# Kernel tuning notes

Measured on AMD Instinct MI355X. Metric: run time of the kernel, lower is better.

Reference implementation:

```python
import jax, jax.numpy as jnp
import numpy as np

SLOPE = 25.0          # fast_sigmoid surrogate slope
H_THRESH = 1.0        # hidden_threshold
O_THRESH = 1.0        # output_threshold
CH_THRESH = 1.0       # cochlea LIF threshold
W_MIN, W_MAX, BITS = 0.001, 1.0, 5

@jax.custom_vjp
def spike(v):
    return (v > 0).astype(v.dtype)

def _spike_fwd(v):
    return spike(v), v

def _spike_bwd(v, g):
    # fast_sigmoid surrogate gradient: 1 / (slope*|v| + 1)^2
    return (g / (SLOPE * jnp.abs(v) + 1.0) ** 2,)

spike.defvjp(_spike_fwd, _spike_bwd)

def fake_quant(w):
    # STE fake quantization (same forward value in train/eval)
    levels = 2 ** BITS
    scale = (W_MAX - W_MIN) / (levels - 1)
    wc = jnp.clip(w, W_MIN, W_MAX)
    q = jnp.round((wc - W_MIN) / scale) * scale + W_MIN
    return wc + jax.lax.stop_gradient(q - wc)

def lif(cur, mem, beta, thresh):
    # snnTorch Leaky, reset_mechanism='subtract': reset from previous mem (detached),
    # then integrate, then fire on new mem.
    reset = jax.lax.stop_gradient(spike(mem - thresh))
    mem = jnp.clip(beta, 0.0, 1.0) * mem + cur - reset * thresh
    spk = spike(mem - thresh)
    return spk, mem

def setup_inputs() -> dict:
    key = jax.random.key(0)
    ks = jax.random.split(key, 8)
    B, T, IN, HID, OUT = 64, 500, 256, 512, 35
    return {
        "x": jax.random.normal(ks[0], (B, T, 1), dtype=jnp.float32),
        "Wch": jax.random.normal(ks[1], (IN, 1), dtype=jnp.float32) * (1.0),
        "W1": jax.random.uniform(ks[2], (HID, IN), minval=W_MIN, maxval=W_MAX, dtype=jnp.float32),
        "W2": jax.random.uniform(ks[3], (HID, HID), minval=W_MIN, maxval=W_MAX, dtype=jnp.float32),
        "W3": jax.random.uniform(ks[4], (HID, HID), minval=W_MIN, maxval=W_MAX, dtype=jnp.float32),
        "W4": jax.random.uniform(ks[5], (OUT, HID), minval=W_MIN, maxval=W_MAX, dtype=jnp.float32),
        "cochlea_betas": jax.random.uniform(ks[6], (IN,), minval=0.05, maxval=0.99, dtype=jnp.float32),
        "beta1": jnp.float32(0.95),
        "beta2": jnp.float32(0.95),
        "beta3": jnp.float32(0.95),
        "beta4": jnp.float32(0.9),
    }

def reference(x, Wch, W1, W2, W3, W4, cochlea_betas, beta1, beta2, beta3, beta4):
    B = x.shape[0]
    # weights are static across time: quantize once, outside the scan
    q1, q2, q3, q4 = fake_quant(W1), fake_quant(W2), fake_quant(W3), fake_quant(W4)
    init = (
        jnp.zeros((B, Wch.shape[0]), x.dtype),  # ch_mem
        jnp.zeros((B, W1.shape[0]), x.dtype),   # mem1
        jnp.zeros((B, W2.shape[0]), x.dtype),   # mem2
        jnp.zeros((B, W3.shape[0]), x.dtype),   # mem3
        jnp.zeros((B, W4.shape[0]), x.dtype),   # mem4
    )

    def step(carry, xt):
        chm, m1, m2, m3, m4 = carry
        ch_spk, chm = lif(xt @ Wch.T, chm, cochlea_betas, CH_THRESH)
        s1, m1 = lif(ch_spk @ q1.T, m1, beta1, H_THRESH)
        s2, m2 = lif(s1 @ q2.T, m2, beta2, H_THRESH)
        s3, m3 = lif(s2 @ q3.T, m3, beta3, H_THRESH)
        s4, m4 = lif(s3 @ q4.T, m4, beta4, O_THRESH)
        return (chm, m1, m2, m3, m4), (s1, s2, s3, s4, m4)

    _, (spk1, spk2, spk3, spk4, mem4) = jax.lax.scan(step, init, jnp.swapaxes(x, 0, 1))
    # each is [T, B, features], matching torch.stack(..., dim=0)
    return spk1, spk2, spk3, spk4, mem4
```

## Files before the change

kernel.cpp:

```cpp
#include <hip/hip_runtime.h>
#include <stdint.h>

#define TT   500
#define BB   64
#define IND  256
#define HD   512
#define OD   35

typedef __attribute__((ext_vector_type(4))) int i32x4;

#define SCALE_F ((float)((1.0 - 0.001) / 31.0))

__device__ __forceinline__ void load16_lds(const int8_t* g, int8_t* l) {
  __builtin_amdgcn_global_load_lds((const __attribute__((address_space(1))) void*)g,
                                   (__attribute__((address_space(3))) void*)l, 16, 0, 0);
}

__global__ __launch_bounds__(256) void k_prep_cochlea(const float* __restrict__ W1,
                                                      const float* __restrict__ W2,
                                                      const float* __restrict__ W3,
                                                      const float* __restrict__ W4,
                                                      int8_t* __restrict__ wk1,
                                                      int8_t* __restrict__ wk2,
                                                      int8_t* __restrict__ wk3,
                                                      int8_t* __restrict__ wk4,
                                                      const float* __restrict__ x,
                                                      const float* __restrict__ Wch,
                                                      const float* __restrict__ cbetas,
                                                      int8_t* __restrict__ chs) {
  __shared__ float xs[TT];
  if (blockIdx.x < 2688) {
    int id = blockIdx.x * 256 + threadIdx.x;
    const float* W; int8_t* wk; int idx, K, H;
    if (id < 131072)       { idx = id;          W = W1; wk = wk1; K = 256; H = 512; }
    else if (id < 393216)  { idx = id - 131072; W = W2; wk = wk2; K = 512; H = 512; }
    else if (id < 655360)  { idx = id - 393216; W = W3; wk = wk3; K = 512; H = 512; }
    else                   { idx = id - 655360; W = W4; wk = wk4; K = 512; H = 35;  }
    int h = idx / K;
    int k = idx - h * K;
    int8_t bits = 0;
    if (h < H) {
      float w  = W[h * K + k];
      float wc = fminf(1.0f, fmaxf(0.001f, w));
      float v  = (wc - 0.001f) / SCALE_F;
      float q  = rintf(v);
      bits = (int8_t)q;
    }
    wk[idx] = bits;
  } else {
    int b = blockIdx.x - 2688;
    int i = threadIdx.x;
    for (int t = threadIdx.x; t < TT; t += 256) xs[t] = x[b * TT + t];
    __syncthreads();
    float w    = Wch[i];
    float beta = fminf(1.0f, fmaxf(0.0f, cbetas[i]));
    float mem  = 0.0f;
    for (int t = 0; t < TT; ++t) {
      float cur = __fmul_rn(xs[t], w);
      int   rs  = (mem > 1.0f);
      float t2  = __fadd_rn(__fmul_rn(beta, mem), cur);
      mem = rs ? __fsub_rn(t2, 1.0f) : t2;
      int spk = (mem > 1.0f);
      chs[(size_t)(t * BB + b) * IND + i] = (int8_t)spk;
    }
  }
}

template<int K>
__device__ __forceinline__ void stage_a(const int8_t* __restrict__ A, int8_t* As,
                                        int b, int gnext, int w, int lane) {
  constexpr int CH = K / 16;
  if (w > 0) {
    constexpr int per = (CH + 2) / 3;
    int jlo = (w - 1) * per, jhi = jlo + per; if (jhi > CH) jhi = CH;
    for (int j = jlo; j < jhi; ++j) {
      int L = j * 64 + lane;
      int r = L / CH, sl = L % CH;
      int kg = (sl - 5 * r) & (CH - 1);
      int t = gnext * 64 + r; if (t > 499) t = 499;
      load16_lds(A + ((size_t)t * 64 + b) * K + kg * 16, &As[j * 1024]);
    }
  }
}

template<int K, bool LAST>
__global__ __launch_bounds__(256, 2) void k_layer(const int8_t* __restrict__ A,
                                                  const int8_t* __restrict__ Bw,
                                                  const float* __restrict__ pbeta,
                                                  float* __restrict__ spk_out,
                                                  int8_t* __restrict__ s_out,
                                                  float* __restrict__ mem_out) {
  constexpr int CH = K / 16;
  constexpr int KS = K / 64;
  __shared__ __align__(16) int8_t Bs[64 * K];
  __shared__ __align__(16) int8_t As[64 * K];
  __shared__ float curbuf[64][64];
  int tid = threadIdx.x, lane = tid & 63, w = tid >> 6;
  int b, h0;
  if (LAST) { b = blockIdx.x;      h0 = 0; }
  else      { b = blockIdx.x & 63; h0 = (blockIdx.x >> 6) * 64; }
  float beta = fminf(1.0f, fmaxf(0.0f, *pbeta));
#pragma unroll
  for (int i = 0; i < CH / 4; ++i) {
    int L = i * 256 + tid;
    int row = L / CH, sl = L % CH;
    int kg = (sl - 5 * row) & (CH - 1);
    load16_lds(Bw + (size_t)(h0 + row) * K + kg * 16, &Bs[(i * 256 + w * 64) * 16]);
  }
  stage_a<K>(A, As, b, 0, w, lane);
  __syncthreads();
  const double DSCALE = (double)SCALE_F;
  const double DWMIN  = (double)0.001f;
  float mem = 0.0f;
  int lr = lane & 15, lk = lane >> 4;
  int arow = w * 16 + lr;
  i32x4 breg[4][KS];
#pragma unroll
  for (int cg = 0; cg < 4; ++cg)
#pragma unroll
    for (int ks = 0; ks < KS; ++ks) {
      int row = cg * 16 + lr;
      int s0 = (ks * 4 + lk + 5 * row) & (CH - 1);
      breg[cg][ks] = *(const i32x4*)&Bs[row * K + s0 * 16];
    }
  const i32x4 ones = {0x01010101, 0x01010101, 0x01010101, 0x01010101};
  for (int g = 0; g < 8; ++g) {
    i32x4 acc0 = {0,0,0,0}, acc1 = {0,0,0,0}, acc2 = {0,0,0,0}, acc3 = {0,0,0,0};
    i32x4 acc4 = {0,0,0,0};
#pragma unroll
    for (int ks = 0; ks < KS; ++ks) {
      int s0 = (ks * 4 + lk + 5 * arow) & (CH - 1);
      i32x4 av = *(const i32x4*)&As[arow * K + s0 * 16];
      acc0 = __builtin_amdgcn_mfma_i32_16x16x64_i8(av, breg[0][ks], acc0, 0, 0, 0);
      acc1 = __builtin_amdgcn_mfma_i32_16x16x64_i8(av, breg[1][ks], acc1, 0, 0, 0);
      acc2 = __builtin_amdgcn_mfma_i32_16x16x64_i8(av, breg[2][ks], acc2, 0, 0, 0);
      acc3 = __builtin_amdgcn_mfma_i32_16x16x64_i8(av, breg[3][ks], acc3, 0, 0, 0);
      acc4 = __builtin_amdgcn_mfma_i32_16x16x64_i8(av, ones, acc4, 0, 0, 0);
    }
    int pr = w * 16 + lk * 4;
#pragma unroll
    for (int i = 0; i < 4; ++i) {
      double nd = (double)acc4[i] * DWMIN;
      curbuf[pr + i][ 0 + lr] = (float)((double)acc0[i] * DSCALE + nd);
      curbuf[pr + i][16 + lr] = (float)((double)acc1[i] * DSCALE + nd);
      curbuf[pr + i][32 + lr] = (float)((double)acc2[i] * DSCALE + nd);
      curbuf[pr + i][48 + lr] = (float)((double)acc3[i] * DSCALE + nd);
    }
    __builtin_amdgcn_sched_barrier(0);
    asm volatile("s_waitcnt lgkmcnt(0)" ::: "memory");
    __builtin_amdgcn_s_barrier();
    __builtin_amdgcn_sched_barrier(0);
    if (g < 7) stage_a<K>(A, As, b, g + 1, w, lane);
    if (w == 0) {
      float curA[16], curB[16];
#define LOADQ(dst, q)                                                         \
      { _Pragma("unroll") for (int r = 0; r < 16; ++r)                        \
          dst[r] = curbuf[(q) * 16 + r][lane]; }
#define CHAINQ(src, q)                                                        \
      { _Pragma("unroll") for (int r = 0; r < 16; ++r) {                      \
          int t = g * 64 + (q) * 16 + r;                                      \
          int   rs = (mem > 1.0f);                                            \
          float t2 = __fadd_rn(__fmul_rn(beta, mem), src[r]);                 \
          mem = rs ? __fsub_rn(t2, 1.0f) : t2;                                \
          int spk = (mem > 1.0f);                                             \
          if (t < 500) {                                                      \
            int row = t * 64 + b;                                             \
            if (!LAST) {                                                      \
              __builtin_nontemporal_store(spk ? 1.0f : 0.0f,                  \
                  &spk_out[(size_t)t * 32768 + (b << 9) + h0 + lane]);        \
              s_out[(size_t)row * 512 + h0 + lane] = (int8_t)spk;             \
            } else if (lane < OD) {                                           \
              __builtin_nontemporal_store(spk ? 1.0f : 0.0f,                  \
                  &spk_out[(size_t)t * (BB * OD) + b * OD + lane]);           \
              __builtin_nontemporal_store(mem,                                \
                  &mem_out[(size_t)t * (BB * OD) + b * OD + lane]);           \
            }                                                                 \
          } } }
      LOADQ(curA, 0)
      LOADQ(curB, 1)
      CHAINQ(curA, 0)
      LOADQ(curA, 2)
      CHAINQ(curB, 1)
      LOADQ(curB, 3)
      CHAINQ(curA, 2)
      CHAINQ(curB, 3)
#undef LOADQ
#undef CHAINQ
    }
    __builtin_amdgcn_sched_barrier(0);
    if (w == 0) asm volatile("s_waitcnt lgkmcnt(0)" ::: "memory");
    else        asm volatile("s_waitcnt vmcnt(0) lgkmcnt(0)" ::: "memory");
    __builtin_amdgcn_s_barrier();
    __builtin_amdgcn_sched_barrier(0);
  }
}

extern "C" void kernel_launch(void* const* d_in, const int* in_sizes, int n_in,
                              void* d_out, int out_size, void* d_ws, size_t ws_size,
                              hipStream_t stream) {
  const float* x      = (const float*)d_in[0];
  const float* Wch    = (const float*)d_in[1];
  const float* W1     = (const float*)d_in[2];
  const float* W2     = (const float*)d_in[3];
  const float* W3     = (const float*)d_in[4];
  const float* W4     = (const float*)d_in[5];
  const float* cbetas = (const float*)d_in[6];
  const float* b1     = (const float*)d_in[7];
  const float* b2     = (const float*)d_in[8];
  const float* b3     = (const float*)d_in[9];
  const float* b4     = (const float*)d_in[10];

  uint8_t* ws = (uint8_t*)d_ws;
  int8_t*   wk1   = (int8_t*)(ws + 0);
  int8_t*   wk2   = (int8_t*)(ws + 131072);
  int8_t*   wk3   = (int8_t*)(ws + 393216);
  int8_t*   wk4   = (int8_t*)(ws + 655360);
  int8_t*   chs   = (int8_t*)(ws + 688128);
  int8_t*   sbufA = (int8_t*)(ws + 8880128);
  int8_t*   sbufB = (int8_t*)(ws + 25264128);

  float* out  = (float*)d_out;
  float* spk1 = out;
  float* spk2 = out + 16384000;
  float* spk3 = out + 32768000;
  float* spk4 = out + 49152000;
  float* mem4 = out + 50272000;

  k_prep_cochlea<<<2752, 256, 0, stream>>>(W1, W2, W3, W4, wk1, wk2, wk3, wk4,
                                           x, Wch, cbetas, chs);

  k_layer<256, false><<<512, 256, 0, stream>>>(chs,   wk1, b1, spk1, sbufA, nullptr);
  k_layer<512, false><<<512, 256, 0, stream>>>(sbufA, wk2, b2, spk2, sbufB, nullptr);
  k_layer<512, false><<<512, 256, 0, stream>>>(sbufB, wk3, b3, spk3, sbufA, nullptr);
  k_layer<512, true ><<<64,  256, 0, stream>>>(sbufA, wk4, b4, spk4, nullptr, mem4);
}
```

Measured before the change: 339.3 us.

## Specialize warps to overlap MFMA, LIF chain, and A-tile loads in layer kernel

The layer kernel grows from 4 to 8 waves and splits them by role. Wave 0 runs the serial LIF recurrence, waves 1-4 each compute a 32x32 MFMA tile of the next time-group's currents, and waves 5-7 prefetch the A tile two groups ahead. Before, the matrix multiply, the chain and the loads ran one after another within each time group. Now the scan of group g overlaps the GEMM of group g+1, at the cost of more barriers per iteration and a single shared current buffer that the barriers must protect.

```diff
diff --git a/kernel.cpp b/kernel.cpp
--- a/kernel.cpp
+++ b/kernel.cpp
@@ -70,21 +70,19 @@
 __device__ __forceinline__ void stage_a(const int8_t* __restrict__ A, int8_t* As,
                                         int b, int gnext, int w, int lane) {
   constexpr int CH = K / 16;
-  if (w > 0) {
-    constexpr int per = (CH + 2) / 3;
-    int jlo = (w - 1) * per, jhi = jlo + per; if (jhi > CH) jhi = CH;
-    for (int j = jlo; j < jhi; ++j) {
-      int L = j * 64 + lane;
-      int r = L / CH, sl = L % CH;
-      int kg = (sl - 5 * r) & (CH - 1);
-      int t = gnext * 64 + r; if (t > 499) t = 499;
-      load16_lds(A + ((size_t)t * 64 + b) * K + kg * 16, &As[j * 1024]);
-    }
+  constexpr int per = (CH + 2) / 3;
+  int jlo = (w - 5) * per, jhi = jlo + per; if (jhi > CH) jhi = CH;
+  for (int j = jlo; j < jhi; ++j) {
+    int L = j * 64 + lane;
+    int r = L / CH, sl = L % CH;
+    int kg = (sl - 5 * r) & (CH - 1);
+    int t = gnext * 64 + r; if (t > 499) t = 499;
+    load16_lds(A + ((size_t)t * 64 + b) * K + kg * 16, &As[j * 1024]);
   }
 }
 
 template<int K, bool LAST>
-__global__ __launch_bounds__(256, 2) void k_layer(const int8_t* __restrict__ A,
+__global__ __launch_bounds__(512, 4) void k_layer(const int8_t* __restrict__ A,
                                                   const int8_t* __restrict__ Bw,
                                                   const float* __restrict__ pbeta,
                                                   float* __restrict__ spk_out,
@@ -94,68 +92,88 @@
   constexpr int KS = K / 64;
   __shared__ __align__(16) int8_t Bs[64 * K];
   __shared__ __align__(16) int8_t As[64 * K];
-  __shared__ float curbuf[64][64];
+  __shared__ float cur[64][64];
   int tid = threadIdx.x, lane = tid & 63, w = tid >> 6;
   int b, h0;
   if (LAST) { b = blockIdx.x;      h0 = 0; }
   else      { b = blockIdx.x & 63; h0 = (blockIdx.x >> 6) * 64; }
   float beta = fminf(1.0f, fmaxf(0.0f, *pbeta));
+  int lr = lane & 15, lk = lane >> 4;
+  const double DSCALE = (double)SCALE_F;
+  const double DWMIN  = (double)0.001f;
+  const i32x4 ones = {0x01010101, 0x01010101, 0x01010101, 0x01010101};
+
 #pragma unroll
-  for (int i = 0; i < CH / 4; ++i) {
-    int L = i * 256 + tid;
+  for (int i = 0; i < K / 128; ++i) {
+    int L = i * 512 + tid;
     int row = L / CH, sl = L % CH;
     int kg = (sl - 5 * row) & (CH - 1);
-    load16_lds(Bw + (size_t)(h0 + row) * K + kg * 16, &Bs[(i * 256 + w * 64) * 16]);
-  }
-  stage_a<K>(A, As, b, 0, w, lane);
+    load16_lds(Bw + (size_t)(h0 + row) * K + kg * 16, &Bs[(i * 512 + w * 64) * 16]);
+  }
+  if (w >= 5) stage_a<K>(A, As, b, 0, w, lane);
   __syncthreads();
-  const double DSCALE = (double)SCALE_F;
-  const double DWMIN  = (double)0.001f;
+
+  int m  = w - 1;
+  int R0 = (m & 1) * 32, C0 = (m >> 1) * 32;
+  i32x4 breg[2][KS];
+  i32x4 acc[2][2], accn[2];
+
+#define MFMA_BATCH()                                                          \
+  { acc[0][0] = (i32x4){0,0,0,0}; acc[0][1] = (i32x4){0,0,0,0};               \
+    acc[1][0] = (i32x4){0,0,0,0}; acc[1][1] = (i32x4){0,0,0,0};               \
+    accn[0]   = (i32x4){0,0,0,0}; accn[1]   = (i32x4){0,0,0,0};               \
+    _Pragma("unroll") for (int ks = 0; ks < KS; ++ks) {                       \
+      int row0 = R0 + lr,      sa0 = (ks*4 + lk + 5*row0) & (CH-1);           \
+      int row1 = R0 + 16 + lr, sa1 = (ks*4 + lk + 5*row1) & (CH-1);           \
+      i32x4 av0 = *(const i32x4*)&As[row0 * K + sa0 * 16];                    \
+      i32x4 av1 = *(const i32x4*)&As[row1 * K + sa1 * 16];                    \
+      acc[0][0] = __builtin_amdgcn_mfma_i32_16x16x64_i8(av0, breg[0][ks], acc[0][0], 0,0,0); \
+      acc[0][1] = __builtin_amdgcn_mfma_i32_16x16x64_i8(av0, breg[1][ks], acc[0][1], 0,0,0); \
+      acc[1][0] = __builtin_amdgcn_mfma_i32_16x16x64_i8(av1, breg[0][ks], acc[1][0], 0,0,0); \
+      acc[1][1] = __builtin_amdgcn_mfma_i32_16x16x64_i8(av1, breg[1][ks], acc[1][1], 0,0,0); \
+      accn[0]   = __builtin_amdgcn_mfma_i32_16x16x64_i8(av0, ones, accn[0], 0,0,0); \
+      accn[1]   = __builtin_amdgcn_mfma_i32_16x16x64_i8(av1, ones, accn[1], 0,0,0); \
+    } }
+
+#define EPI()                                                                 \
+  { _Pragma("unroll") for (int rf = 0; rf < 2; ++rf) {                        \
+      int pr = R0 + rf * 16 + lk * 4;                                         \
+      _Pragma("unroll") for (int i = 0; i < 4; ++i) {                         \
+        double nd = (double)accn[rf][i] * DWMIN;                              \
+        cur[pr + i][C0 +  0 + lr] = (float)((double)acc[rf][0][i] * DSCALE + nd); \
+        cur[pr + i][C0 + 16 + lr] = (float)((double)acc[rf][1][i] * DSCALE + nd); \
+      } } }
+
+  if (w >= 1 && w <= 4) {
+#pragma unroll
+    for (int cf = 0; cf < 2; ++cf)
+#pragma unroll
+      for (int ks = 0; ks < KS; ++ks) {
+        int row = C0 + cf * 16 + lr;
+        int s0 = (ks * 4 + lk + 5 * row) & (CH - 1);
+        breg[cf][ks] = *(const i32x4*)&Bs[row * K + s0 * 16];
+      }
+    MFMA_BATCH()
+  }
+  __builtin_amdgcn_sched_barrier(0);
+  asm volatile("s_waitcnt lgkmcnt(0)" ::: "memory");
+  __builtin_amdgcn_s_barrier();
+  __builtin_amdgcn_sched_barrier(0);
+  if (w >= 1 && w <= 4) EPI()
+  if (w >= 5) stage_a<K>(A, As, b, 1, w, lane);
+  __builtin_amdgcn_sched_barrier(0);
+  if (w >= 5) asm volatile("s_waitcnt vmcnt(0) lgkmcnt(0)" ::: "memory");
+  else        asm volatile("s_waitcnt lgkmcnt(0)" ::: "memory");
+  __builtin_amdgcn_s_barrier();
+  __builtin_amdgcn_sched_barrier(0);
+
   float mem = 0.0f;
-  int lr = lane & 15, lk = lane >> 4;
-  int arow = w * 16 + lr;
-  i32x4 breg[4][KS];
-#pragma unroll
-  for (int cg = 0; cg < 4; ++cg)
-#pragma unroll
-    for (int ks = 0; ks < KS; ++ks) {
-      int row = cg * 16 + lr;
-      int s0 = (ks * 4 + lk + 5 * row) & (CH - 1);
-      breg[cg][ks] = *(const i32x4*)&Bs[row * K + s0 * 16];
-    }
-  const i32x4 ones = {0x01010101, 0x01010101, 0x01010101, 0x01010101};
   for (int g = 0; g < 8; ++g) {
-    i32x4 acc0 = {0,0,0,0}, acc1 = {0,0,0,0}, acc2 = {0,0,0,0}, acc3 = {0,0,0,0};
-    i32x4 acc4 = {0,0,0,0};
-#pragma unroll
-    for (int ks = 0; ks < KS; ++ks) {
-      int s0 = (ks * 4 + lk + 5 * arow) & (CH - 1);
-      i32x4 av = *(const i32x4*)&As[arow * K + s0 * 16];
-      acc0 = __builtin_amdgcn_mfma_i32_16x16x64_i8(av, breg[0][ks], acc0, 0, 0, 0);
-      acc1 = __builtin_amdgcn_mfma_i32_16x16x64_i8(av, breg[1][ks], acc1, 0, 0, 0);
-      acc2 = __builtin_amdgcn_mfma_i32_16x16x64_i8(av, breg[2][ks], acc2, 0, 0, 0);
-      acc3 = __builtin_amdgcn_mfma_i32_16x16x64_i8(av, breg[3][ks], acc3, 0, 0, 0);
-      acc4 = __builtin_amdgcn_mfma_i32_16x16x64_i8(av, ones, acc4, 0, 0, 0);
-    }
-    int pr = w * 16 + lk * 4;
-#pragma unroll
-    for (int i = 0; i < 4; ++i) {
-      double nd = (double)acc4[i] * DWMIN;
-      curbuf[pr + i][ 0 + lr] = (float)((double)acc0[i] * DSCALE + nd);
-      curbuf[pr + i][16 + lr] = (float)((double)acc1[i] * DSCALE + nd);
-      curbuf[pr + i][32 + lr] = (float)((double)acc2[i] * DSCALE + nd);
-      curbuf[pr + i][48 + lr] = (float)((double)acc3[i] * DSCALE + nd);
-    }
-    __builtin_amdgcn_sched_barrier(0);
-    asm volatile("s_waitcnt lgkmcnt(0)" ::: "memory");
-    __builtin_amdgcn_s_barrier();
-    __builtin_amdgcn_sched_barrier(0);
-    if (g < 7) stage_a<K>(A, As, b, g + 1, w, lane);
     if (w == 0) {
       float curA[16], curB[16];
 #define LOADQ(dst, q)                                                         \
       { _Pragma("unroll") for (int r = 0; r < 16; ++r)                        \
-          dst[r] = curbuf[(q) * 16 + r][lane]; }
+          dst[r] = cur[(q) * 16 + r][lane]; }
 #define CHAINQ(src, q)                                                        \
       { _Pragma("unroll") for (int r = 0; r < 16; ++r) {                      \
           int t = g * 64 + (q) * 16 + r;                                      \
@@ -186,13 +204,23 @@
       CHAINQ(curB, 3)
 #undef LOADQ
 #undef CHAINQ
+    } else if (w <= 4 && g < 7) {
+      MFMA_BATCH()
     }
     __builtin_amdgcn_sched_barrier(0);
-    if (w == 0) asm volatile("s_waitcnt lgkmcnt(0)" ::: "memory");
-    else        asm volatile("s_waitcnt vmcnt(0) lgkmcnt(0)" ::: "memory");
+    asm volatile("s_waitcnt lgkmcnt(0)" ::: "memory");
     __builtin_amdgcn_s_barrier();
     __builtin_amdgcn_sched_barrier(0);
-  }
+    if (w >= 1 && w <= 4 && g < 7) EPI()
+    if (w >= 5 && g < 6) stage_a<K>(A, As, b, g + 2, w, lane);
+    __builtin_amdgcn_sched_barrier(0);
+    if (w >= 5) asm volatile("s_waitcnt vmcnt(0) lgkmcnt(0)" ::: "memory");
+    else        asm volatile("s_waitcnt lgkmcnt(0)" ::: "memory");
+    __builtin_amdgcn_s_barrier();
+    __builtin_amdgcn_sched_barrier(0);
+  }
+#undef MFMA_BATCH
+#undef EPI
 }
 
 extern "C" void kernel_launch(void* const* d_in, const int* in_sizes, int n_in,
@@ -229,8 +257,8 @@
   k_prep_cochlea<<<2752, 256, 0, stream>>>(W1, W2, W3, W4, wk1, wk2, wk3, wk4,
                                            x, Wch, cbetas, chs);
 
-  k_layer<256, false><<<512, 256, 0, stream>>>(chs,   wk1, b1, spk1, sbufA, nullptr);
-  k_layer<512, false><<<512, 256, 0, stream>>>(sbufA, wk2, b2, spk2, sbufB, nullptr);
-  k_layer<512, false><<<512, 256, 0, stream>>>(sbufB, wk3, b3, spk3, sbufA, nullptr);
-  k_layer<512, true ><<<64,  256, 0, stream>>>(sbufA, wk4, b4, spk4, nullptr, mem4);
-}
+  k_layer<256, false><<<512, 512, 0, stream>>>(chs,   wk1, b1, spk1, sbufA, nullptr);
+  k_layer<512, false><<<512, 512, 0, stream>>>(sbufA, wk2, b2, spk2, sbufB, nullptr);
+  k_layer<512, false><<<512, 512, 0, stream>>>(sbufB, wk3, b3, spk3, sbufA, nullptr);
+  k_layer<512, true ><<<64,  512, 0, stream>>>(sbufA, wk4, b4, spk4, nullptr, mem4);
+}
```

Result: slower. 370.0 us (+9.0%).
